# Kernel tuning notes

Measured on AMD Instinct MI355X. Metric: run time of the kernel, lower is better.

The kernel has to match this reference:

```python
import jax, jax.numpy as jnp
import numpy as np
import math

B, L, D = 2, 2048, 256
N_SETS, PLANES_PER_SET = 4, 4
TOTAL_PLANES = N_SETS * PLANES_PER_SET  # 16
POS_PLANES = 16
LTM_PLANES = POS_PLANES
PI = math.pi
LN_EPS = 1e-5


def _mlp2(x, w1, b1, w2, b2):
    h = jax.nn.gelu(x @ w1 + b1, approximate=False)  # torch nn.GELU default = erf
    return h @ w2 + b2


def setup_inputs() -> dict:
    key = jax.random.key(0)
    ks = iter(jax.random.split(key, 40))
    def W(shape):
        return jax.random.normal(next(ks), shape, jnp.float32) / np.float32(np.sqrt(shape[0]))
    z = lambda *s: jnp.zeros(s, jnp.float32)
    return dict(
        x=jax.random.normal(next(ks), (B, L, D), jnp.float32),
        ke_w1=W((D, D)), ke_b1=z(D), ke_w2=W((D, TOTAL_PLANES)), ke_b2=z(TOTAL_PLANES),
        qe_w1=W((D, D)), qe_b1=z(D), qe_w2=W((D, TOTAL_PLANES)), qe_b2=z(TOTAL_PLANES),
        v_w=W((D, D)), v_b=z(D),
        out_ln_g=jnp.ones(D, jnp.float32), out_ln_b=z(D),
        out_w=W((D, D)), out_b=z(D),
        set_weights=jnp.ones(N_SETS, jnp.float32),
        pos_weight=jnp.ones((), jnp.float32),
        gate_w1=W((D, D // 2)), gate_b1=z(D // 2), gate_w2=W((D // 2, 1)), gate_b2=z(1),
        lke_w1=W((D, D)), lke_b1=z(D), lke_w2=W((D, LTM_PLANES)), lke_b2=z(LTM_PLANES),
        surprise_scale=jnp.asarray(5.0, jnp.float32), surprise_bias=jnp.asarray(0.0, jnp.float32),
        resonance_scale=jnp.asarray(5.0, jnp.float32), resonance_threshold=jnp.asarray(0.3, jnp.float32),
        ltm_weight=jnp.asarray(0.5, jnp.float32),
        pos_freqs=jnp.exp(jnp.arange(POS_PLANES, dtype=jnp.float32) * (-math.log(10000.0) / POS_PLANES)),
        ltm_binding_mem=((jax.random.normal(next(ks), (LTM_PLANES, D))
                          + 1j * jax.random.normal(next(ks), (LTM_PLANES, D))) * 0.5).astype(jnp.complex64),
        ltm_count=jnp.asarray(100.0, jnp.float32),
    )


def reference(x, ke_w1, ke_b1, ke_w2, ke_b2, qe_w1, qe_b1, qe_w2, qe_b2,
              v_w, v_b, out_ln_g, out_ln_b, out_w, out_b,
              set_weights, pos_weight, gate_w1, gate_b1, gate_w2, gate_b2,
              lke_w1, lke_b1, lke_w2, lke_b2,
              surprise_scale, surprise_bias, resonance_scale, resonance_threshold,
              ltm_weight, pos_freqs, ltm_binding_mem, ltm_count):
    B_, L_, D_ = x.shape
    key_phasor = jnp.exp(1j * (jnp.tanh(_mlp2(x, ke_w1, ke_b1, ke_w2, ke_b2)) * PI))    # (B,L,16) complex64
    query_phasor = jnp.exp(1j * (jnp.tanh(_mlp2(x, qe_w1, qe_b1, qe_w2, qe_b2)) * PI))  # (B,L,16)
    kp = key_phasor.reshape(B_, L_, N_SETS, PLANES_PER_SET)
    qp = query_phasor.reshape(B_, L_, N_SETS, PLANES_PER_SET)
    weights = jax.nn.softmax(set_weights)
    V_real = x @ v_w + v_b                                                              # (B,L,D)

    # --- cross-bank surprise gate (n_sets > 1 branch) ---
    joint_key = jnp.prod(kp, axis=2)    # (B,L,PP)
    joint_query = jnp.prod(qp, axis=2)
    km = jnp.cumsum(joint_key, axis=1)
    key_memory = jnp.concatenate([jnp.zeros_like(km[:, :1]), km[:, :-1]], axis=1)       # shifted cumsum
    resonance_mag = jnp.abs(key_memory * jnp.conj(joint_query)).mean(-1, keepdims=True)
    positions = jnp.maximum(jnp.arange(L_, dtype=x.dtype), 1.0)
    norm_res = resonance_mag / jnp.sqrt(positions)[None, :, None]
    scale = jnp.clip(resonance_scale, 1.0, 20.0)
    thr = jnp.clip(resonance_threshold, 0.1, 0.9)
    surprise = 0.5 * (1.0 - jnp.tanh(scale * (norm_res - thr)))
    write_gate = jax.nn.sigmoid(surprise_scale * (surprise - 0.5) + surprise_bias)      # (B,L,1)
    Vg = (V_real * write_gate).astype(jnp.complex64)

    # --- cross-bank retrieval over joint (product) phasors ---
    bound = joint_key[..., None] * Vg[:, :, None, :]                                     # (B,L,PP,D)
    mem = jnp.cumsum(bound, axis=1)
    cross = jnp.real((mem * jnp.conj(joint_query)[..., None]).sum(2))                    # (B,L,D)

    # --- per-bank retrieval over all 16 planes ---
    bound_all = key_phasor[..., None] * Vg[:, :, None, :]                                # (B,L,16,D)
    mem_all = jnp.cumsum(bound_all, axis=1)
    ret_all = mem_all * jnp.conj(query_phasor)[..., None]
    per_bank = jnp.real(ret_all.reshape(B_, L_, N_SETS, PLANES_PER_SET, D_).sum(3))      # (B,L,S,D)
    total = (per_bank * weights[None, None, :, None]).sum(2)
    total = (total + cross) / (N_SETS + 1)

    # --- positional phase plane ---
    pos_phase = jnp.arange(L_, dtype=x.dtype)[:, None] * pos_freqs * (2.0 * PI)          # (L,16)
    pos_phasor = jnp.exp(1j * pos_phase)
    Vc = V_real.astype(jnp.complex64)
    bound_pos = pos_phasor[None, :, :, None] * Vc[:, :, None, :]                         # (B,L,16,D)
    mem_pos = jnp.cumsum(bound_pos, axis=1)
    ret_pos = jnp.real((mem_pos * jnp.conj(pos_phasor)[None, :, :, None]).sum(2))        # (B,L,D)
    gate = jax.nn.sigmoid(_mlp2(x, gate_w1, gate_b1, gate_w2, gate_b2))                  # (B,L,1)
    total = gate * total + (1.0 - gate) * (jax.nn.sigmoid(pos_weight) * ret_pos)

    # --- long-term memory retrieval (inference path; buffers are constants) ---
    ltm_phasor = jnp.exp(1j * (jnp.tanh(_mlp2(x, lke_w1, lke_b1, lke_w2, lke_b2)) * PI)) # (B,L,16)
    persistent = jnp.real((ltm_binding_mem[None, None] * jnp.conj(ltm_phasor)[..., None]).sum(2))
    pnorm = jnp.sqrt(jnp.maximum(ltm_count, 1.0) * LTM_PLANES)
    total = total + jax.nn.sigmoid(ltm_weight) * (persistent / pnorm)

    # --- to_out: LayerNorm + Linear ---
    mu = total.mean(-1, keepdims=True)
    var = ((total - mu) ** 2).mean(-1, keepdims=True)
    h = (total - mu) / jnp.sqrt(var + LN_EPS) * out_ln_g + out_ln_b
    return h @ out_w + out_b
```

## Files before the change

### kernel.cpp

```cpp
#include <hip/hip_runtime.h>
#include <hip/hip_bf16.h>
#include <math.h>

#define BB 2
#define LL 2048
#define DD 256
#define NT (BB*LL)
#define HCOLS 896
#define NCOLS 1152
#define KBIG 768
#define FDIM 80
#define CC 64
#define NC (NT/CC)
#define NCB (LL/CC)
#define SST (FDIM*DD)
#define PI_F 3.14159265358979323846f

typedef __attribute__((ext_vector_type(8))) short s8frag;
typedef __attribute__((ext_vector_type(4))) float f4acc;

#define GLDS16(g, l) __builtin_amdgcn_global_load_lds( \
    (const __attribute__((address_space(1))) void*)(g), \
    (__attribute__((address_space(3))) void*)(l), 16, 0, 0)

__device__ __forceinline__ float gelu_erf(float v) {
    return 0.5f * v * (1.0f + erff(v * 0.70710678118654752440f));
}
__device__ __forceinline__ float sigmoidf_(float v) {
    return 1.0f / (1.0f + expf(-v));
}

#define K0A_BLKS (NT * DD / 4 / 256)
#define K0B_BLKS ((KBIG / 64) * (NCOLS / 64))
#define K0C_BLKS (4 * 16 * 768 / 256)
#define K0D_BLKS 5
__global__ __launch_bounds__(256) void k0_prep(
    const float* __restrict__ x,
    const float* __restrict__ ke_w1, const float* __restrict__ ke_b1,
    const float* __restrict__ qe_w1, const float* __restrict__ qe_b1,
    const float* __restrict__ lke_w1, const float* __restrict__ lke_b1,
    const float* __restrict__ gate_w1, const float* __restrict__ gate_b1,
    const float* __restrict__ v_w, const float* __restrict__ v_b,
    const float* __restrict__ ke_w2, const float* __restrict__ qe_w2,
    const float* __restrict__ lke_w2, const float* __restrict__ gate_w2,
    __hip_bfloat16* __restrict__ xhi, __hip_bfloat16* __restrict__ xlo,
    __hip_bfloat16* __restrict__ BT, float* __restrict__ bcat,
    __hip_bfloat16* __restrict__ W2T)
{
    __shared__ float tile[64][65];
    const int b = blockIdx.x, tid = threadIdx.x;
    if (b < K0A_BLKS) {
        int idx = b * 256 + tid;
        float4 v = reinterpret_cast<const float4*>(x)[idx];
        float vv[4] = {v.x, v.y, v.z, v.w};
        #pragma unroll
        for (int j = 0; j < 4; ++j) {
            __hip_bfloat16 h = __float2bfloat16(vv[j]);
            xhi[idx * 4 + j] = h;
            xlo[idx * 4 + j] = __float2bfloat16(vv[j] - __bfloat162float(h));
        }
    } else if (b < K0A_BLKS + K0B_BLKS) {
        int bb = b - K0A_BLKS;
        int bk = bb / 18, bn = bb - bk * 18;
        int kp0 = bk * 64, n0 = bn * 64;
        int seg = kp0 >> 8;
        int k0 = kp0 - seg * 256;
        #pragma unroll 4
        for (int i = 0; i < 16; ++i) {
            int kl = i * 4 + (tid >> 6);
            int nl = tid & 63;
            int k = k0 + kl, n = n0 + nl;
            float w;
            if (n < 256)      w = ke_w1[k * 256 + n];
            else if (n < 512) w = qe_w1[k * 256 + (n - 256)];
            else if (n < 768) w = lke_w1[k * 256 + (n - 512)];
            else if (n < 896) w = gate_w1[k * 128 + (n - 768)];
            else              w = v_w[k * 256 + (n - 896)];
            tile[kl][nl] = w;
        }
        __syncthreads();
        #pragma unroll 4
        for (int i = 0; i < 16; ++i) {
            int nl = i * 4 + (tid >> 6);
            int kpl = tid & 63;
            float w = tile[kpl][nl];
            __hip_bfloat16 hi = __float2bfloat16(w);
            __hip_bfloat16 out = (seg == 1)
                ? __float2bfloat16(w - __bfloat162float(hi)) : hi;
            BT[(size_t)(n0 + nl) * KBIG + kp0 + kpl] = out;
        }
    } else if (b < K0A_BLKS + K0B_BLKS + K0C_BLKS) {
        int idx = (b - K0A_BLKS - K0B_BLKS) * 256 + tid;
        int g = idx / (16 * 768);
        int rem = idx - g * (16 * 768);
        int n = rem / 768;
        int kp = rem - n * 768;
        float w = 0.0f;
        int seg;
        if (g < 3) {
            seg = kp >> 8;
            int k = kp & 255;
            const float* W = (g == 0) ? ke_w2 : (g == 1) ? qe_w2 : lke_w2;
            w = W[k * 16 + n];
        } else {
            seg = kp >> 7;
            int k = kp & 127;
            if (n == 0 && kp < 384) w = gate_w2[k];
            else { seg = 0; w = 0.0f; }
        }
        __hip_bfloat16 hi = __float2bfloat16(w);
        __hip_bfloat16 out = (seg == 1) ? __float2bfloat16(w - __bfloat162float(hi)) : hi;
        W2T[idx] = out;
    } else {
        int n = (b - K0A_BLKS - K0B_BLKS - K0C_BLKS) * 256 + tid;
        if (n < NCOLS) {
            float bia;
            if (n < 256)      bia = ke_b1[n];
            else if (n < 512) bia = qe_b1[n - 256];
            else if (n < 768) bia = lke_b1[n - 512];
            else if (n < 896) bia = gate_b1[n - 768];
            else              bia = v_b[n - 896];
            bcat[n] = bia;
        }
    }
}

__global__ __launch_bounds__(256) void k1_mfma(
    const __hip_bfloat16* __restrict__ xhi, const __hip_bfloat16* __restrict__ xlo,
    const __hip_bfloat16* __restrict__ BT, const float* __restrict__ bcat,
    __hip_bfloat16* __restrict__ Hhi, __hip_bfloat16* __restrict__ Hlo,
    float* __restrict__ V)
{
    __shared__ __align__(16) short As[128 * 64];
    __shared__ __align__(16) short Bs[64 * 64];
    const int tid = threadIdx.x;
    const int wave = tid >> 6, lane = tid & 63;
    const int wr = wave >> 1, wc = wave & 1;
    const int bm = blockIdx.x, bn = blockIdx.y;
    const int lg = lane >> 4, lr = lane & 15;

    f4acc acc[4][2] = {};

    for (int kt = 0; kt < KBIG / 64; ++kt) {
        const int k0 = kt * 64;
        const __hip_bfloat16* xsrc = (kt < 8) ? xhi : xlo;
        const int kcol = (kt < 8) ? (k0 & 255) : (k0 - 512);
        #pragma unroll
        for (int j = 0; j < 4; ++j) {
            int r0 = wave * 32 + j * 8;
            int row = r0 + (lane >> 3);
            int ch = (lane & 7) ^ (row & 7);
            GLDS16(xsrc + (size_t)(bm * 128 + row) * DD + kcol + ch * 8, &As[r0 * 64]);
        }
        #pragma unroll
        for (int j = 0; j < 2; ++j) {
            int r0 = wave * 16 + j * 8;
            int row = r0 + (lane >> 3);
            int ch = (lane & 7) ^ (row & 7);
            GLDS16(BT + (size_t)(bn * 64 + row) * KBIG + k0 + ch * 8, &Bs[r0 * 64]);
        }
        __syncthreads();
        #pragma unroll
        for (int kk = 0; kk < 2; ++kk) {
            s8frag a[4], b[2];
            #pragma unroll
            for (int i = 0; i < 4; ++i) {
                int arow = wr * 64 + i * 16 + lr;
                int slot = (kk * 4 + lg) ^ (arow & 7);
                a[i] = *reinterpret_cast<const s8frag*>(&As[arow * 64 + slot * 8]);
            }
            #pragma unroll
            for (int i = 0; i < 2; ++i) {
                int brow = wc * 32 + i * 16 + lr;
                int slot = (kk * 4 + lg) ^ (brow & 7);
                b[i] = *reinterpret_cast<const s8frag*>(&Bs[brow * 64 + slot * 8]);
            }
            #pragma unroll
            for (int mi = 0; mi < 4; ++mi)
                #pragma unroll
                for (int ni = 0; ni < 2; ++ni)
                    acc[mi][ni] = __builtin_amdgcn_mfma_f32_16x16x32_bf16(
                        a[mi], b[ni], acc[mi][ni], 0, 0, 0);
        }
        __syncthreads();
    }

    #pragma unroll
    for (int ni = 0; ni < 2; ++ni) {
        int n = bn * 64 + wc * 32 + ni * 16 + lr;
        float bia = bcat[n];
        #pragma unroll
        for (int mi = 0; mi < 4; ++mi) {
            #pragma unroll
            for (int r = 0; r < 4; ++r) {
                int m = bm * 128 + wr * 64 + mi * 16 + lg * 4 + r;
                float v = acc[mi][ni][r] + bia;
                if (n < HCOLS) {
                    float hv = gelu_erf(v);
                    __hip_bfloat16 h = __float2bfloat16(hv);
                    Hhi[(size_t)m * HCOLS + n] = h;
                    Hlo[(size_t)m * HCOLS + n] = __float2bfloat16(hv - __bfloat162float(h));
                } else {
                    V[(size_t)m * DD + (n - HCOLS)] = v;
                }
            }
        }
    }
}

__global__ __launch_bounds__(256) void k2_fused(
    const __hip_bfloat16* __restrict__ Hhi, const __hip_bfloat16* __restrict__ Hlo,
    const __hip_bfloat16* __restrict__ W2T,
    const float* __restrict__ ke_b2, const float* __restrict__ qe_b2,
    const float* __restrict__ lke_b2, const float* __restrict__ gate_b2,
    const float* __restrict__ set_weights, const float* __restrict__ pos_weight,
    const float* __restrict__ ltm_weight, const float* __restrict__ ltm_count,
    const float* __restrict__ pos_freqs,
    float* __restrict__ Fk, float* __restrict__ Fq, float* __restrict__ Fql,
    float* __restrict__ J)
{
    __shared__ float c2s[32][52];
    const int tid = threadIdx.x;
    const int g = tid >> 6, lane = tid & 63;
    const int lg = lane >> 4, lr = lane & 15;
    const int t0 = blockIdx.x * 32;

    {
        const int seglen = (g < 3) ? 256 : 128;
        const int gbase = (g < 3) ? g * 256 : 768;
        const int nsteps = (g < 3) ? 24 : 12;
        const __hip_bfloat16* wbase = W2T + (size_t)(g * 16 + lr) * 768;
        f4acc acc[2] = {};
        for (int kt = 0; kt < nsteps; ++kt) {
            const int kp = kt * 32;
            const int seg = kp / seglen;
            const int kk = kp - seg * seglen;
            const __hip_bfloat16* asrc = (seg < 2) ? Hhi : Hlo;
            const int col = gbase + kk + lg * 8;
            s8frag b = *reinterpret_cast<const s8frag*>(wbase + kp + lg * 8);
            #pragma unroll
            for (int mi = 0; mi < 2; ++mi) {
                s8frag a = *reinterpret_cast<const s8frag*>(
                    asrc + (size_t)(t0 + mi * 16 + lr) * HCOLS + col);
                acc[mi] = __builtin_amdgcn_mfma_f32_16x16x32_bf16(a, b, acc[mi], 0, 0, 0);
            }
        }
        int col = g * 16 + lr;
        if (col < 49) {
            #pragma unroll
            for (int mi = 0; mi < 2; ++mi)
                #pragma unroll
                for (int r = 0; r < 4; ++r)
                    c2s[mi * 16 + lg * 4 + r][col] = acc[mi][r];
        }
    }
    __syncthreads();

    for (int i = tid; i < 32 * 64; i += 256) {
        int t = i >> 6, c = i & 63;
        if (c < 49) {
            float a = c2s[t][c];
            float val;
            if (c < 16)      val = tanhf(a + ke_b2[c]) * PI_F;
            else if (c < 32) val = tanhf(a + qe_b2[c - 16]) * PI_F;
            else if (c < 48) val = tanhf(a + lke_b2[c - 32]) * PI_F;
            else             val = sigmoidf_(a + gate_b2[0]);
            c2s[t][c] = val;
        }
    }
    __syncthreads();

    float sw[4];
    {
        float s0 = set_weights[0], s1 = set_weights[1], s2 = set_weights[2], s3 = set_weights[3];
        float mx = fmaxf(fmaxf(s0, s1), fmaxf(s2, s3));
        float e0 = expf(s0 - mx), e1 = expf(s1 - mx), e2 = expf(s2 - mx), e3 = expf(s3 - mx);
        float inv = 1.0f / (e0 + e1 + e2 + e3);
        sw[0] = e0 * inv; sw[1] = e1 * inv; sw[2] = e2 * inv; sw[3] = e3 * inv;
    }
    const float spw = sigmoidf_(pos_weight[0]);
    const float altm = sigmoidf_(ltm_weight[0]) / sqrtf(fmaxf(ltm_count[0], 1.0f) * 16.0f);
    const int sg = tid >> 5, sl = tid & 31;

    for (int tr = 0; tr < 4; ++tr) {
        const int lt = tr * 8 + sg;
        const int t = t0 + lt;
        const float gg = c2s[lt][48];
        const float aq = gg * 0.2f;
        const float apos = (1.0f - gg) * spw;
        const int l = t & (LL - 1);
        float* fkr  = Fk  + (size_t)t * FDIM;
        float* fqr  = Fq  + (size_t)t * FDIM;
        float* fqlr = Fql + (size_t)t * 32;

        if (sl < 16) {
            int p = sl;
            float sk, ck; sincosf(c2s[lt][p], &sk, &ck);
            fkr[2 * p] = ck; fkr[2 * p + 1] = sk;
            float sq, cq; sincosf(c2s[lt][16 + p], &sq, &cq);
            float wq = aq * sw[p >> 2];
            fqr[2 * p] = wq * cq; fqr[2 * p + 1] = wq * sq;
            float sl_, cl_; sincosf(c2s[lt][32 + p], &sl_, &cl_);
            fqlr[2 * p] = altm * cl_; fqlr[2 * p + 1] = altm * sl_;
            float th = (float)l * pos_freqs[p] * (2.0f * PI_F);
            float sp, cp; sincosf(th, &sp, &cp);
            fkr[40 + 2 * p] = cp; fkr[41 + 2 * p] = sp;
            fqr[40 + 2 * p] = apos * cp; fqr[41 + 2 * p] = apos * sp;
        } else if (sl < 20) {
            int p = sl - 16;
            float pjk = c2s[lt][p] + c2s[lt][p + 4] + c2s[lt][p + 8] + c2s[lt][p + 12];
            float pjq = c2s[lt][16 + p] + c2s[lt][20 + p] + c2s[lt][24 + p] + c2s[lt][28 + p];
            float sjk, cjk; sincosf(pjk, &sjk, &cjk);
            float sjq, cjq; sincosf(pjq, &sjq, &cjq);
            fkr[32 + 2 * p] = cjk; fkr[33 + 2 * p] = sjk;
            fqr[32 + 2 * p] = aq * cjq; fqr[33 + 2 * p] = aq * sjq;
            J[(size_t)(2 * p) * NT + t] = cjk;
            J[(size_t)(2 * p + 1) * NT + t] = sjk;
        } else if (sl < 24) {
            int p = sl - 20;
            fkr[72 + 2 * p] = 0.0f; fkr[73 + 2 * p] = 0.0f;
            fqr[72 + 2 * p] = 0.0f; fqr[73 + 2 * p] = 0.0f;
        }
    }
}

__device__ __forceinline__ int swz2048(int l) {
    return (l & ~31) | ((l ^ (l >> 5)) & 31);
}
__global__ __launch_bounds__(512) void k3a_scan(
    const float* __restrict__ J, float* __restrict__ wg,
    const float* __restrict__ resonance_scale, const float* __restrict__ resonance_threshold,
    const float* __restrict__ surprise_scale, const float* __restrict__ surprise_bias)
{
    __shared__ float km[8 * LL];
    const int b = blockIdx.x;
    const int tid = threadIdx.x;
    const int w = tid >> 6;
    const int lane = tid & 63;
    {
        float v[32];
        float s = 0.0f;
        int l0 = lane * 32;
        const float4* src = reinterpret_cast<const float4*>(
            J + (size_t)w * NT + b * LL + l0);
        #pragma unroll
        for (int i = 0; i < 8; ++i) {
            float4 q = src[i];
            v[4 * i + 0] = q.x; v[4 * i + 1] = q.y;
            v[4 * i + 2] = q.z; v[4 * i + 3] = q.w;
            s += q.x + q.y + q.z + q.w;
        }
        float local = s;
        #pragma unroll
        for (int off = 1; off < 64; off <<= 1) {
            float n = __shfl_up(s, off);
            if (lane >= off) s += n;
        }
        float run = s - local;
        #pragma unroll 4
        for (int i = 0; i < 32; ++i) { km[w * LL + swz2048(l0 + i)] = run; run += v[i]; }
    }
    __syncthreads();
    const float sc  = fminf(fmaxf(resonance_scale[0], 1.0f), 20.0f);
    const float th  = fminf(fmaxf(resonance_threshold[0], 0.1f), 0.9f);
    const float ssc = surprise_scale[0];
    const float sbi = surprise_bias[0];
    for (int q = 0; q < 4; ++q) {
        int l = tid + 512 * q;
        int ls = swz2048(l);
        float rm = 0.0f;
        #pragma unroll
        for (int p = 0; p < 4; ++p) {
            float re = km[(2 * p) * LL + ls], im = km[(2 * p + 1) * LL + ls];
            rm += sqrtf(re * re + im * im);
        }
        rm *= 0.25f;
        float nr = rm / sqrtf(fmaxf((float)l, 1.0f));
        float sur = 0.5f * (1.0f - tanhf(sc * (nr - th)));
        wg[b * LL + l] = sigmoidf_(ssc * (sur - 0.5f) + sbi);
    }
}

__global__ __launch_bounds__(256) void k4a_state(
    const float* __restrict__ Fk, const float* __restrict__ wg,
    const float* __restrict__ V, float* __restrict__ S)
{
    __shared__ __align__(16) float fk[CC][FDIM];
    const int c = blockIdx.x;
    const int f0 = blockIdx.y * 20;
    const int tid = threadIdx.x;
    for (int i = tid; i < CC * FDIM; i += 256) {
        int r = i / FDIM, cx = i - r * FDIM;
        float f = Fk[(size_t)c * CC * FDIM + i];
        if (cx < 40) f *= wg[c * CC + r];
        fk[r][cx] = f;
    }
    __syncthreads();
    float acc[20];
    #pragma unroll
    for (int f = 0; f < 20; ++f) acc[f] = 0.0f;
    const float* vp = V + (size_t)c * CC * DD + tid;
    for (int r = 0; r < CC; ++r) {
        float v = vp[(size_t)r * DD];
        #pragma unroll
        for (int g = 0; g < 5; ++g) {
            float4 q = *reinterpret_cast<const float4*>(&fk[r][f0 + 4 * g]);
            acc[4 * g + 0] += q.x * v; acc[4 * g + 1] += q.y * v;
            acc[4 * g + 2] += q.z * v; acc[4 * g + 3] += q.w * v;
        }
    }
    float* sp = S + (size_t)c * SST + tid;
    #pragma unroll
    for (int f = 0; f < 20; ++f) sp[(size_t)(f0 + f) * DD] = acc[f];
}

__global__ __launch_bounds__(256) void k4b_scan(
    const float* __restrict__ S, float* __restrict__ M)
{
    const int e = blockIdx.x * 256 + threadIdx.x;
    const int b = blockIdx.y;
    float run = 0.0f;
    #pragma unroll 8
    for (int cc = 0; cc < NCB; ++cc) {
        size_t o = ((size_t)(b * NCB + cc)) * SST + e;
        M[o] = run;
        run += S[o];
    }
}

__global__ __launch_bounds__(256) void k4c_fused(
    const float* __restrict__ Fq, const float* __restrict__ Fk,
    const float* __restrict__ wg, const float* __restrict__ Fql,
    const float* __restrict__ V, const float* __restrict__ M,
    const float* __restrict__ ltm_mem,
    const float* __restrict__ gln, const float* __restrict__ bln,
    const float* __restrict__ out_w, const float* __restrict__ out_b,
    float* __restrict__ out)
{
    __shared__ __align__(16) float fq[8][FDIM];
    __shared__ __align__(16) float fkS[CC * 96];
    __shared__ __align__(16) float sc[8][68];
    const int c = blockIdx.x;
    const int h = blockIdx.y;
    const int r0 = h * 8;
    const int nrows = r0 + 8;
    const int tid = threadIdx.x;
    const int wave = tid >> 6, lane = tid & 63;

    for (int i = tid; i < 8 * FDIM; i += 256) {
        int r = i / FDIM, cx = i - r * FDIM;
        fq[r][cx] = Fq[(size_t)(c * CC + r0 + r) * FDIM + cx];
    }
    for (int i = tid; i < nrows * FDIM; i += 256) {
        int r = i / FDIM, cx = i - r * FDIM;
        float f = Fk[(size_t)c * CC * FDIM + i];
        if (cx < 40) f *= wg[c * CC + r];
        fkS[r * 96 + (cx ^ ((r & 7) << 2))] = f;
    }
    __syncthreads();

    #pragma unroll
    for (int q = 0; q < 2; ++q) {
        int idx = tid + 256 * q;
        int i = idx >> 6, j = idx & 63;
        float s = 0.0f;
        if (r0 + i >= j) {
            const int sw = (j & 7) << 2;
            #pragma unroll
            for (int g = 0; g < 20; ++g) {
                float4 a = *reinterpret_cast<const float4*>(&fq[i][4 * g]);
                float4 b = *reinterpret_cast<const float4*>(&fkS[j * 96 + ((4 * g) ^ sw)]);
                s += a.x * b.x + a.y * b.y + a.z * b.z + a.w * b.w;
            }
        }
        sc[i][j] = s;
    }
    __syncthreads();

    const int d = tid;
    float acc[8];
    #pragma unroll
    for (int i = 0; i < 8; ++i) acc[i] = 0.0f;

    const float* mp = M + (size_t)c * SST + d;
    #pragma unroll 2
    for (int g = 0; g < 20; ++g) {
        float m0 = mp[(size_t)(4 * g + 0) * DD];
        float m1 = mp[(size_t)(4 * g + 1) * DD];
        float m2 = mp[(size_t)(4 * g + 2) * DD];
        float m3 = mp[(size_t)(4 * g + 3) * DD];
        #pragma unroll
        for (int i = 0; i < 8; ++i) {
            float4 a = *reinterpret_cast<const float4*>(&fq[i][4 * g]);
            acc[i] += a.x * m0 + a.y * m1 + a.z * m2 + a.w * m3;
        }
    }
    const float* vp = V + (size_t)c * CC * DD + d;
    const int j4max = nrows >> 2;
    #pragma unroll 2
    for (int j4 = 0; j4 < j4max; ++j4) {
        float v0 = vp[(size_t)(4 * j4 + 0) * DD];
        float v1 = vp[(size_t)(4 * j4 + 1) * DD];
        float v2 = vp[(size_t)(4 * j4 + 2) * DD];
        float v3 = vp[(size_t)(4 * j4 + 3) * DD];
        #pragma unroll
        for (int i = 0; i < 8; ++i) {
            float4 s4 = *reinterpret_cast<const float4*>(&sc[i][4 * j4]);
            acc[i] += s4.x * v0 + s4.y * v1 + s4.z * v2 + s4.w * v3;
        }
    }
    {
        float mre[16], mim[16];
        #pragma unroll
        for (int p = 0; p < 16; ++p) {
            mre[p] = ltm_mem[((size_t)p * DD + d) * 2];
            mim[p] = ltm_mem[((size_t)p * DD + d) * 2 + 1];
        }
        __syncthreads();
        {
            int r = tid >> 5, p = tid & 31;
            sc[r][p] = Fql[(size_t)(c * CC + r0 + r) * 32 + p];
        }
        __syncthreads();
        #pragma unroll
        for (int i = 0; i < 8; ++i) {
            float a = acc[i];
            #pragma unroll
            for (int p = 0; p < 16; ++p)
                a += sc[i][2 * p] * mre[p] + sc[i][2 * p + 1] * mim[p];
            acc[i] = a;
        }
    }
    __syncthreads();

    #pragma unroll
    for (int i = 0; i < 8; ++i) {
        float s = acc[i], s2 = acc[i] * acc[i];
        #pragma unroll
        for (int off = 1; off < 64; off <<= 1) {
            s  += __shfl_xor(s, off);
            s2 += __shfl_xor(s2, off);
        }
        if (lane == 0) { sc[i][wave] = s; sc[i][4 + wave] = s2; }
    }
    __syncthreads();
    const float gv = gln[d], bv = bln[d];
    #pragma unroll
    for (int i = 0; i < 8; ++i) {
        float s  = sc[i][0] + sc[i][1] + sc[i][2] + sc[i][3];
        float s2 = sc[i][4] + sc[i][5] + sc[i][6] + sc[i][7];
        float mu = s * (1.0f / 256.0f);
        float var = s2 * (1.0f / 256.0f) - mu * mu;
        float rstd = rsqrtf(var + 1e-5f);
        fkS[i * 256 + d] = (acc[i] - mu) * rstd * gv + bv;
    }
    __syncthreads();

    float oacc[8];
    #pragma unroll
    for (int i = 0; i < 8; ++i) oacc[i] = 0.0f;
    #pragma unroll 2
    for (int d0 = 0; d0 < DD; d0 += 4) {
        float w0 = out_w[(size_t)(d0 + 0) * DD + tid];
        float w1 = out_w[(size_t)(d0 + 1) * DD + tid];
        float w2 = out_w[(size_t)(d0 + 2) * DD + tid];
        float w3 = out_w[(size_t)(d0 + 3) * DD + tid];
        #pragma unroll
        for (int i = 0; i < 8; ++i) {
            float4 hq = *reinterpret_cast<const float4*>(&fkS[i * 256 + d0]);
            oacc[i] += hq.x * w0 + hq.y * w1 + hq.z * w2 + hq.w * w3;
        }
    }
    float ob = out_b[tid];
    float* op = out + (size_t)(c * CC + r0) * DD + tid;
    #pragma unroll
    for (int i = 0; i < 8; ++i)
        op[(size_t)i * DD] = oacc[i] + ob;
}

extern "C" void kernel_launch(void* const* d_in, const int* in_sizes, int n_in,
                              void* d_out, int out_size, void* d_ws, size_t ws_size,
                              hipStream_t stream)
{
    (void)in_sizes; (void)n_in; (void)out_size; (void)ws_size;
    const float* x        = (const float*)d_in[0];
    const float* ke_w1    = (const float*)d_in[1];
    const float* ke_b1    = (const float*)d_in[2];
    const float* ke_w2    = (const float*)d_in[3];
    const float* ke_b2    = (const float*)d_in[4];
    const float* qe_w1    = (const float*)d_in[5];
    const float* qe_b1    = (const float*)d_in[6];
    const float* qe_w2    = (const float*)d_in[7];
    const float* qe_b2    = (const float*)d_in[8];
    const float* v_w      = (const float*)d_in[9];
    const float* v_b      = (const float*)d_in[10];
    const float* out_ln_g = (const float*)d_in[11];
    const float* out_ln_b = (const float*)d_in[12];
    const float* out_w    = (const float*)d_in[13];
    const float* out_b    = (const float*)d_in[14];
    const float* set_weights = (const float*)d_in[15];
    const float* pos_weight  = (const float*)d_in[16];
    const float* gate_w1  = (const float*)d_in[17];
    const float* gate_b1  = (const float*)d_in[18];
    const float* gate_w2  = (const float*)d_in[19];
    const float* gate_b2  = (const float*)d_in[20];
    const float* lke_w1   = (const float*)d_in[21];
    const float* lke_b1   = (const float*)d_in[22];
    const float* lke_w2   = (const float*)d_in[23];
    const float* lke_b2   = (const float*)d_in[24];
    const float* surprise_scale      = (const float*)d_in[25];
    const float* surprise_bias       = (const float*)d_in[26];
    const float* resonance_scale     = (const float*)d_in[27];
    const float* resonance_threshold = (const float*)d_in[28];
    const float* ltm_weight = (const float*)d_in[29];
    const float* pos_freqs  = (const float*)d_in[30];
    const float* ltm_mem    = (const float*)d_in[31];
    const float* ltm_count  = (const float*)d_in[32];

    float* ws  = (float*)d_ws;
    float* Hf  = ws;
    float* V   = Hf  + (size_t)NT * HCOLS;
    float* Fk  = V   + (size_t)NT * DD;
    float* Fq  = Fk  + (size_t)NT * FDIM;
    float* Fql = Fq  + (size_t)NT * FDIM;
    float* Tot = Fql + (size_t)NT * 32;
    float* J   = Tot + (size_t)NT * DD;
    __hip_bfloat16* W2T = (__hip_bfloat16*)(J + (size_t)NT * 8);
    float* wg  = (float*)(W2T + 4 * 16 * 768);

    __hip_bfloat16* Hhi = (__hip_bfloat16*)Hf;
    __hip_bfloat16* Hlo = Hhi + (size_t)NT * HCOLS;
    float* S   = Hf;
    float* M   = Hf + (size_t)NC * SST;
    __hip_bfloat16* xhi = (__hip_bfloat16*)Fk;
    __hip_bfloat16* xlo = xhi + (size_t)NT * DD;
    __hip_bfloat16* BT  = xlo + (size_t)NT * DD;
    float* bcat = (float*)(BT + (size_t)NCOLS * KBIG);

    k0_prep<<<K0A_BLKS + K0B_BLKS + K0C_BLKS + K0D_BLKS, 256, 0, stream>>>(
        x, ke_w1, ke_b1, qe_w1, qe_b1, lke_w1, lke_b1, gate_w1, gate_b1, v_w, v_b,
        ke_w2, qe_w2, lke_w2, gate_w2, xhi, xlo, BT, bcat, W2T);
    k1_mfma<<<dim3(NT / 128, NCOLS / 64), 256, 0, stream>>>(xhi, xlo, BT, bcat,
                                                            Hhi, Hlo, V);
    k2_fused<<<NT / 32, 256, 0, stream>>>(Hhi, Hlo, W2T,
                                          ke_b2, qe_b2, lke_b2, gate_b2,
                                          set_weights, pos_weight,
                                          ltm_weight, ltm_count, pos_freqs,
                                          Fk, Fq, Fql, J);
    k3a_scan<<<BB, 512, 0, stream>>>(J, wg, resonance_scale, resonance_threshold,
                                     surprise_scale, surprise_bias);
    k4a_state<<<dim3(NC, 4), 256, 0, stream>>>(Fk, wg, V, S);
    k4b_scan<<<dim3(SST / 256, BB), 256, 0, stream>>>(S, M);
    k4c_fused<<<dim3(NC, 8), 256, 0, stream>>>(Fq, Fk, wg, Fql, V, M, ltm_mem,
                                               out_ln_g, out_ln_b, out_w, out_b,
                                               (float*)d_out);
}
```

Baseline: 132.8 us.

## Split output projection into LayerNorm pass and split-bf16 MFMA GEMM

The fused retrieval kernel no longer does LayerNorm and the fp32 scalar output projection. It now writes the pre-norm totals to a workspace buffer and processes 16 rows per block instead of 8. A separate LayerNorm kernel writes hi/lo bf16 splits, and a new MFMA GEMM kernel applies out_w, which the prep kernel pre-splits and transposes. This replaces the slow per-thread fp32 matvec with matrix cores, at the cost of two extra launches and an extra round trip of the totals through memory.

```diff
diff --git a/kernel.cpp b/kernel.cpp
--- a/kernel.cpp
+++ b/kernel.cpp
@@ -29,9 +29,13 @@
 __device__ __forceinline__ float sigmoidf_(float v) {
     return 1.0f / (1.0f + expf(-v));
 }
+__device__ __forceinline__ unsigned short bf16bits(__hip_bfloat16 h) {
+    return *reinterpret_cast<unsigned short*>(&h);
+}
 
 #define K0A_BLKS (NT * DD / 4 / 256)
-#define K0B_BLKS ((KBIG / 64) * (NCOLS / 64))
+#define K0B_TW   22
+#define K0B_BLKS ((KBIG / 64) * K0B_TW)
 #define K0C_BLKS (4 * 16 * 768 / 256)
 #define K0D_BLKS 5
 __global__ __launch_bounds__(256) void k0_prep(
@@ -43,9 +47,10 @@
     const float* __restrict__ v_w, const float* __restrict__ v_b,
     const float* __restrict__ ke_w2, const float* __restrict__ qe_w2,
     const float* __restrict__ lke_w2, const float* __restrict__ gate_w2,
+    const float* __restrict__ out_w,
     __hip_bfloat16* __restrict__ xhi, __hip_bfloat16* __restrict__ xlo,
     __hip_bfloat16* __restrict__ BT, float* __restrict__ bcat,
-    __hip_bfloat16* __restrict__ W2T)
+    __hip_bfloat16* __restrict__ W2T, __hip_bfloat16* __restrict__ OWT)
 {
     __shared__ float tile[64][65];
     const int b = blockIdx.x, tid = threadIdx.x;
@@ -61,7 +66,7 @@
         }
     } else if (b < K0A_BLKS + K0B_BLKS) {
         int bb = b - K0A_BLKS;
-        int bk = bb / 18, bn = bb - bk * 18;
+        int bk = bb / K0B_TW, bn = bb - bk * K0B_TW;
         int kp0 = bk * 64, n0 = bn * 64;
         int seg = kp0 >> 8;
         int k0 = kp0 - seg * 256;
@@ -71,11 +76,12 @@
             int nl = tid & 63;
             int k = k0 + kl, n = n0 + nl;
             float w;
-            if (n < 256)      w = ke_w1[k * 256 + n];
-            else if (n < 512) w = qe_w1[k * 256 + (n - 256)];
-            else if (n < 768) w = lke_w1[k * 256 + (n - 512)];
-            else if (n < 896) w = gate_w1[k * 128 + (n - 768)];
-            else              w = v_w[k * 256 + (n - 896)];
+            if (n < 256)       w = ke_w1[k * 256 + n];
+            else if (n < 512)  w = qe_w1[k * 256 + (n - 256)];
+            else if (n < 768)  w = lke_w1[k * 256 + (n - 512)];
+            else if (n < 896)  w = gate_w1[k * 128 + (n - 768)];
+            else if (n < 1152) w = v_w[k * 256 + (n - 896)];
+            else               w = out_w[k * 256 + (n - 1152)];
             tile[kl][nl] = w;
         }
         __syncthreads();
@@ -87,7 +93,10 @@
             __hip_bfloat16 hi = __float2bfloat16(w);
             __hip_bfloat16 out = (seg == 1)
                 ? __float2bfloat16(w - __bfloat162float(hi)) : hi;
-            BT[(size_t)(n0 + nl) * KBIG + kp0 + kpl] = out;
+            if (n0 < 1152)
+                BT[(size_t)(n0 + nl) * KBIG + kp0 + kpl] = out;
+            else
+                OWT[(size_t)(n0 + nl - 1152) * KBIG + kp0 + kpl] = out;
         }
     } else if (b < K0A_BLKS + K0B_BLKS + K0C_BLKS) {
         int idx = (b - K0A_BLKS - K0B_BLKS) * 256 + tid;
@@ -428,26 +437,22 @@
     }
 }
 
-__global__ __launch_bounds__(256) void k4c_fused(
+__global__ __launch_bounds__(256) void k4c_out(
     const float* __restrict__ Fq, const float* __restrict__ Fk,
     const float* __restrict__ wg, const float* __restrict__ Fql,
     const float* __restrict__ V, const float* __restrict__ M,
-    const float* __restrict__ ltm_mem,
-    const float* __restrict__ gln, const float* __restrict__ bln,
-    const float* __restrict__ out_w, const float* __restrict__ out_b,
-    float* __restrict__ out)
-{
-    __shared__ __align__(16) float fq[8][FDIM];
+    const float* __restrict__ ltm_mem, float* __restrict__ Tot)
+{
+    __shared__ __align__(16) float fq[16][FDIM];
     __shared__ __align__(16) float fkS[CC * 96];
-    __shared__ __align__(16) float sc[8][68];
+    __shared__ __align__(16) float sc[16][68];
     const int c = blockIdx.x;
     const int h = blockIdx.y;
-    const int r0 = h * 8;
-    const int nrows = r0 + 8;
+    const int r0 = h * 16;
+    const int nrows = r0 + 16;
     const int tid = threadIdx.x;
-    const int wave = tid >> 6, lane = tid & 63;
-
-    for (int i = tid; i < 8 * FDIM; i += 256) {
+
+    for (int i = tid; i < 16 * FDIM; i += 256) {
         int r = i / FDIM, cx = i - r * FDIM;
         fq[r][cx] = Fq[(size_t)(c * CC + r0 + r) * FDIM + cx];
     }
@@ -460,7 +465,7 @@
     __syncthreads();
 
     #pragma unroll
-    for (int q = 0; q < 2; ++q) {
+    for (int q = 0; q < 4; ++q) {
         int idx = tid + 256 * q;
         int i = idx >> 6, j = idx & 63;
         float s = 0.0f;
@@ -478,9 +483,9 @@
     __syncthreads();
 
     const int d = tid;
-    float acc[8];
-    #pragma unroll
-    for (int i = 0; i < 8; ++i) acc[i] = 0.0f;
+    float acc[16];
+    #pragma unroll
+    for (int i = 0; i < 16; ++i) acc[i] = 0.0f;
 
     const float* mp = M + (size_t)c * SST + d;
     #pragma unroll 2
@@ -490,7 +495,7 @@
         float m2 = mp[(size_t)(4 * g + 2) * DD];
         float m3 = mp[(size_t)(4 * g + 3) * DD];
         #pragma unroll
-        for (int i = 0; i < 8; ++i) {
+        for (int i = 0; i < 16; ++i) {
             float4 a = *reinterpret_cast<const float4*>(&fq[i][4 * g]);
             acc[i] += a.x * m0 + a.y * m1 + a.z * m2 + a.w * m3;
         }
@@ -504,78 +509,153 @@
         float v2 = vp[(size_t)(4 * j4 + 2) * DD];
         float v3 = vp[(size_t)(4 * j4 + 3) * DD];
         #pragma unroll
-        for (int i = 0; i < 8; ++i) {
+        for (int i = 0; i < 16; ++i) {
             float4 s4 = *reinterpret_cast<const float4*>(&sc[i][4 * j4]);
             acc[i] += s4.x * v0 + s4.y * v1 + s4.z * v2 + s4.w * v3;
         }
     }
-    {
-        float mre[16], mim[16];
-        #pragma unroll
-        for (int p = 0; p < 16; ++p) {
-            mre[p] = ltm_mem[((size_t)p * DD + d) * 2];
-            mim[p] = ltm_mem[((size_t)p * DD + d) * 2 + 1];
+    float mre[16], mim[16];
+    #pragma unroll
+    for (int p = 0; p < 16; ++p) {
+        mre[p] = ltm_mem[((size_t)p * DD + d) * 2];
+        mim[p] = ltm_mem[((size_t)p * DD + d) * 2 + 1];
+    }
+    __syncthreads();
+    for (int i = tid; i < 16 * 32; i += 256) {
+        int r = i >> 5, p = i & 31;
+        sc[r][p] = Fql[(size_t)(c * CC + r0 + r) * 32 + p];
+    }
+    __syncthreads();
+    float* tp = Tot + (size_t)(c * CC + r0) * DD + d;
+    #pragma unroll 1
+    for (int i = 0; i < 16; ++i) {
+        float a = acc[i];
+        #pragma unroll
+        for (int p = 0; p < 16; ++p)
+            a += sc[i][2 * p] * mre[p] + sc[i][2 * p + 1] * mim[p];
+        tp[(size_t)i * DD] = a;
+    }
+}
+
+__global__ __launch_bounds__(256) void k5a_ln(
+    const float* __restrict__ Tot,
+    const float* __restrict__ gln, const float* __restrict__ bln,
+    __hip_bfloat16* __restrict__ Hnhi, __hip_bfloat16* __restrict__ Hnlo)
+{
+    const int tid = threadIdx.x;
+    const int t0 = blockIdx.x * 16;
+    const int w = tid >> 6, lane = tid & 63;
+    const int r = 4 * w + (lane >> 4);
+    const int l4 = lane & 15;
+    const int t = t0 + r;
+    float vbuf[16];
+    float s = 0.0f, s2 = 0.0f;
+    const float4* src = reinterpret_cast<const float4*>(
+        Tot + (size_t)t * DD + l4 * 16);
+    #pragma unroll
+    for (int g = 0; g < 4; ++g) {
+        float4 v = src[g];
+        vbuf[4 * g + 0] = v.x; vbuf[4 * g + 1] = v.y;
+        vbuf[4 * g + 2] = v.z; vbuf[4 * g + 3] = v.w;
+        s += v.x + v.y + v.z + v.w;
+        s2 += v.x * v.x + v.y * v.y + v.z * v.z + v.w * v.w;
+    }
+    #pragma unroll
+    for (int off = 1; off < 16; off <<= 1) {
+        s  += __shfl_xor(s, off);
+        s2 += __shfl_xor(s2, off);
+    }
+    float mu = s * (1.0f / 256.0f);
+    float var = s2 * (1.0f / 256.0f) - mu * mu;
+    float rstd = rsqrtf(var + 1e-5f);
+    unsigned hw[8], lw[8];
+    #pragma unroll
+    for (int j = 0; j < 8; ++j) {
+        unsigned short h0, h1, l0, l1;
+        #pragma unroll
+        for (int e = 0; e < 2; ++e) {
+            int i = 2 * j + e;
+            int k = l4 * 16 + i;
+            float hn = (vbuf[i] - mu) * rstd * gln[k] + bln[k];
+            __hip_bfloat16 hb = __float2bfloat16(hn);
+            __hip_bfloat16 lb = __float2bfloat16(hn - __bfloat162float(hb));
+            if (e == 0) { h0 = bf16bits(hb); l0 = bf16bits(lb); }
+            else        { h1 = bf16bits(hb); l1 = bf16bits(lb); }
+        }
+        hw[j] = (unsigned)h0 | ((unsigned)h1 << 16);
+        lw[j] = (unsigned)l0 | ((unsigned)l1 << 16);
+    }
+    uint4* dh = reinterpret_cast<uint4*>(Hnhi + (size_t)t * DD + l4 * 16);
+    uint4* dl = reinterpret_cast<uint4*>(Hnlo + (size_t)t * DD + l4 * 16);
+    dh[0] = make_uint4(hw[0], hw[1], hw[2], hw[3]);
+    dh[1] = make_uint4(hw[4], hw[5], hw[6], hw[7]);
+    dl[0] = make_uint4(lw[0], lw[1], lw[2], lw[3]);
+    dl[1] = make_uint4(lw[4], lw[5], lw[6], lw[7]);
+}
+
+__global__ __launch_bounds__(256) void k5b_mfma(
+    const __hip_bfloat16* __restrict__ Hnhi, const __hip_bfloat16* __restrict__ Hnlo,
+    const __hip_bfloat16* __restrict__ OWT, const float* __restrict__ out_b,
+    float* __restrict__ out)
+{
+    __shared__ __align__(16) short As[64 * 64];
+    __shared__ __align__(16) short Bs[64 * 64];
+    const int tid = threadIdx.x;
+    const int wave = tid >> 6, lane = tid & 63;
+    const int wr = wave >> 1, wc = wave & 1;
+    const int bm = blockIdx.x, bn = blockIdx.y;
+    const int lg = lane >> 4, lr = lane & 15;
+
+    f4acc acc[2][2] = {};
+
+    for (int kt = 0; kt < KBIG / 64; ++kt) {
+        const int k0 = kt * 64;
+        const __hip_bfloat16* asrc = (kt < 8) ? Hnhi : Hnlo;
+        const int kcol = (kt < 8) ? (k0 & 255) : (k0 - 512);
+        #pragma unroll
+        for (int j = 0; j < 2; ++j) {
+            int r0 = wave * 16 + j * 8;
+            int row = r0 + (lane >> 3);
+            int ch = (lane & 7) ^ (row & 7);
+            GLDS16(asrc + (size_t)(bm * 64 + row) * DD + kcol + ch * 8, &As[r0 * 64]);
+            GLDS16(OWT + (size_t)(bn * 64 + row) * KBIG + k0 + ch * 8, &Bs[r0 * 64]);
         }
         __syncthreads();
-        {
-            int r = tid >> 5, p = tid & 31;
-            sc[r][p] = Fql[(size_t)(c * CC + r0 + r) * 32 + p];
+        #pragma unroll
+        for (int kk = 0; kk < 2; ++kk) {
+            s8frag a[2], b[2];
+            #pragma unroll
+            for (int i = 0; i < 2; ++i) {
+                int arow = wr * 32 + i * 16 + lr;
+                int aslot = (kk * 4 + lg) ^ (arow & 7);
+                a[i] = *reinterpret_cast<const s8frag*>(&As[arow * 64 + aslot * 8]);
+                int brow = wc * 32 + i * 16 + lr;
+                int bslot = (kk * 4 + lg) ^ (brow & 7);
+                b[i] = *reinterpret_cast<const s8frag*>(&Bs[brow * 64 + bslot * 8]);
+            }
+            #pragma unroll
+            for (int mi = 0; mi < 2; ++mi)
+                #pragma unroll
+                for (int ni = 0; ni < 2; ++ni)
+                    acc[mi][ni] = __builtin_amdgcn_mfma_f32_16x16x32_bf16(
+                        a[mi], b[ni], acc[mi][ni], 0, 0, 0);
         }
         __syncthreads();
-        #pragma unroll
-        for (int i = 0; i < 8; ++i) {
-            float a = acc[i];
-            #pragma unroll
-            for (int p = 0; p < 16; ++p)
-                a += sc[i][2 * p] * mre[p] + sc[i][2 * p + 1] * mim[p];
-            acc[i] = a;
-        }
-    }
-    __syncthreads();
-
-    #pragma unroll
-    for (int i = 0; i < 8; ++i) {
-        float s = acc[i], s2 = acc[i] * acc[i];
-        #pragma unroll
-        for (int off = 1; off < 64; off <<= 1) {
-            s  += __shfl_xor(s, off);
-            s2 += __shfl_xor(s2, off);
-        }
-        if (lane == 0) { sc[i][wave] = s; sc[i][4 + wave] = s2; }
-    }
-    __syncthreads();
-    const float gv = gln[d], bv = bln[d];
-    #pragma unroll
-    for (int i = 0; i < 8; ++i) {
-        float s  = sc[i][0] + sc[i][1] + sc[i][2] + sc[i][3];
-        float s2 = sc[i][4] + sc[i][5] + sc[i][6] + sc[i][7];
-        float mu = s * (1.0f / 256.0f);
-        float var = s2 * (1.0f / 256.0f) - mu * mu;
-        float rstd = rsqrtf(var + 1e-5f);
-        fkS[i * 256 + d] = (acc[i] - mu) * rstd * gv + bv;
-    }
-    __syncthreads();
-
-    float oacc[8];
-    #pragma unroll
-    for (int i = 0; i < 8; ++i) oacc[i] = 0.0f;
-    #pragma unroll 2
-    for (int d0 = 0; d0 < DD; d0 += 4) {
-        float w0 = out_w[(size_t)(d0 + 0) * DD + tid];
-        float w1 = out_w[(size_t)(d0 + 1) * DD + tid];
-        float w2 = out_w[(size_t)(d0 + 2) * DD + tid];
-        float w3 = out_w[(size_t)(d0 + 3) * DD + tid];
-        #pragma unroll
-        for (int i = 0; i < 8; ++i) {
-            float4 hq = *reinterpret_cast<const float4*>(&fkS[i * 256 + d0]);
-            oacc[i] += hq.x * w0 + hq.y * w1 + hq.z * w2 + hq.w * w3;
-        }
-    }
-    float ob = out_b[tid];
-    float* op = out + (size_t)(c * CC + r0) * DD + tid;
-    #pragma unroll
-    for (int i = 0; i < 8; ++i)
-        op[(size_t)i * DD] = oacc[i] + ob;
+    }
+
+    #pragma unroll
+    for (int ni = 0; ni < 2; ++ni) {
+        int n = bn * 64 + wc * 32 + ni * 16 + lr;
+        float ob = out_b[n];
+        #pragma unroll
+        for (int mi = 0; mi < 2; ++mi) {
+            #pragma unroll
+            for (int r = 0; r < 4; ++r) {
+                int m = bm * 64 + wr * 32 + mi * 16 + lg * 4 + r;
+                out[(size_t)m * DD + n] = acc[mi][ni][r] + ob;
+            }
+        }
+    }
 }
 
 extern "C" void kernel_launch(void* const* d_in, const int* in_sizes, int n_in,
@@ -627,11 +707,14 @@
     float* J   = Tot + (size_t)NT * DD;
     __hip_bfloat16* W2T = (__hip_bfloat16*)(J + (size_t)NT * 8);
     float* wg  = (float*)(W2T + 4 * 16 * 768);
+    __hip_bfloat16* OWT = (__hip_bfloat16*)(wg + NT);
 
     __hip_bfloat16* Hhi = (__hip_bfloat16*)Hf;
     __hip_bfloat16* Hlo = Hhi + (size_t)NT * HCOLS;
     float* S   = Hf;
     float* M   = Hf + (size_t)NC * SST;
+    __hip_bfloat16* Hnhi = (__hip_bfloat16*)Hf;
+    __hip_bfloat16* Hnlo = Hnhi + (size_t)NT * DD;
     __hip_bfloat16* xhi = (__hip_bfloat16*)Fk;
     __hip_bfloat16* xlo = xhi + (size_t)NT * DD;
     __hip_bfloat16* BT  = xlo + (size_t)NT * DD;
@@ -639,7 +722,7 @@
 
     k0_prep<<<K0A_BLKS + K0B_BLKS + K0C_BLKS + K0D_BLKS, 256, 0, stream>>>(
         x, ke_w1, ke_b1, qe_w1, qe_b1, lke_w1, lke_b1, gate_w1, gate_b1, v_w, v_b,
-        ke_w2, qe_w2, lke_w2, gate_w2, xhi, xlo, BT, bcat, W2T);
+        ke_w2, qe_w2, lke_w2, gate_w2, out_w, xhi, xlo, BT, bcat, W2T, OWT);
     k1_mfma<<<dim3(NT / 128, NCOLS / 64), 256, 0, stream>>>(xhi, xlo, BT, bcat,
                                                             Hhi, Hlo, V);
     k2_fused<<<NT / 32, 256, 0, stream>>>(Hhi, Hlo, W2T,
@@ -651,7 +734,8 @@
                                      surprise_scale, surprise_bias);
     k4a_state<<<dim3(NC, 4), 256, 0, stream>>>(Fk, wg, V, S);
     k4b_scan<<<dim3(SST / 256, BB), 256, 0, stream>>>(S, M);
-    k4c_fused<<<dim3(NC, 8), 256, 0, stream>>>(Fq, Fk, wg, Fql, V, M, ltm_mem,
-                                               out_ln_g, out_ln_b, out_w, out_b,
-                                               (float*)d_out);
-}
+    k4c_out<<<dim3(NC, 4), 256, 0, stream>>>(Fq, Fk, wg, Fql, V, M, ltm_mem, Tot);
+    k5a_ln<<<NT / 16, 256, 0, stream>>>(Tot, out_ln_g, out_ln_b, Hnhi, Hnlo);
+    k5b_mfma<<<dim3(NT / 64, DD / 64), 256, 0, stream>>>(Hnhi, Hnlo, OWT, out_b,
+                                                         (float*)d_out);
+}
```

After: 123.6 us. 1.07x faster.
